# Performance work log

Hardware: AMD Instinct MI355X
Metric: run time of the kernel (lower is better)

## Reference

```python
import jax, jax.numpy as jnp
import numpy as np

N = 50000      # nodes
E = 800000     # edges (before self-loops)
F_IN = 256     # nfeat
HEADS = 8      # nhead
C1 = 16        # hidden_sizes (per-head channels of conv1)
NCLS = 40      # nclass
NEG_SLOPE = 0.2


def setup_inputs() -> dict:
    key = jax.random.key(0)
    ks = jax.random.split(key, 12)
    s = 0.1
    x = jax.random.normal(ks[0], (N, F_IN), dtype=jnp.float32)
    edge_index = jax.random.randint(ks[1], (2, E), 0, N, dtype=jnp.int64)
    edge_attr = jax.random.normal(ks[2], (E,), dtype=jnp.float32)  # unused by forward
    W1 = jax.random.normal(ks[3], (F_IN, HEADS * C1), dtype=jnp.float32) * s
    att_src1 = jax.random.normal(ks[4], (HEADS, C1), dtype=jnp.float32) * s
    att_dst1 = jax.random.normal(ks[5], (HEADS, C1), dtype=jnp.float32) * s
    b1 = jnp.zeros((HEADS * C1,), dtype=jnp.float32)
    W2 = jax.random.normal(ks[6], (HEADS * C1, NCLS), dtype=jnp.float32) * s
    att_src2 = jax.random.normal(ks[7], (1, NCLS), dtype=jnp.float32) * s
    att_dst2 = jax.random.normal(ks[8], (1, NCLS), dtype=jnp.float32) * s
    b2 = jnp.zeros((NCLS,), dtype=jnp.float32)
    return {"x": x, "edge_index": edge_index, "edge_attr": edge_attr,
            "W1": W1, "att_src1": att_src1, "att_dst1": att_dst1, "b1": b1,
            "W2": W2, "att_src2": att_src2, "att_dst2": att_dst2, "b2": b2}


def gat_layer(x, W, att_src, att_dst, bias, src, dst, concat):
    """PyG-style GATConv (eval mode, no dropout). src/dst include self-loops."""
    H, C = att_src.shape
    h = (x @ W).reshape(-1, H, C)                     # [N,H,C]
    a_src = (h * att_src[None]).sum(-1)               # [N,H]
    a_dst = (h * att_dst[None]).sum(-1)               # [N,H]
    e = jax.nn.leaky_relu(a_src[src] + a_dst[dst], NEG_SLOPE)  # [Etot,H]
    # segment softmax over destination neighborhoods
    m = jax.ops.segment_max(e, dst, num_segments=N)   # [N,H]
    m = jax.lax.stop_gradient(jnp.where(jnp.isfinite(m), m, 0.0))
    p = jnp.exp(e - m[dst])
    denom = jax.ops.segment_sum(p, dst, num_segments=N)
    alpha = p / (denom[dst] + 1e-16)                  # [Etot,H]
    out = jax.ops.segment_sum(alpha[:, :, None] * h[src], dst, num_segments=N)  # [N,H,C]
    out = out.reshape(-1, H * C) if concat else out.mean(axis=1)
    return out + bias


def reference(x, edge_index, edge_attr, W1, att_src1, att_dst1, b1, W2, att_src2, att_dst2, b2):
    # add self loops (PyG GATConv default)
    loops = jnp.arange(N, dtype=edge_index.dtype)
    src = jnp.concatenate([edge_index[0], loops])
    dst = jnp.concatenate([edge_index[1], loops])
    # eval mode: F.dropout is identity
    h = jax.nn.elu(gat_layer(x, W1, att_src1, att_dst1, b1, src, dst, concat=True))
    final = gat_layer(h, W2, att_src2, att_dst2, b2, src, dst, concat=False)
    return final, jax.nn.log_softmax(final, axis=1)
```

## Files before the change

### kernel.cpp

```cpp
#include <hip/hip_runtime.h>

#define NN 50000
#define EE 800000
#define FIN 256
#define HD 8
#define C1 16
#define HC 128
#define NC 40
#define NEG 0.2f
#define CAP 64
#define R2 32
#define BM 64
#define GB1 ((NN + BM - 1) / BM)
#define NP_N (NN / 8)
#define SCB 2048

typedef __attribute__((ext_vector_type(8))) short short8;
typedef __attribute__((ext_vector_type(4))) float f32x4;
union FragU { uint4 u; short8 s; };

__device__ __forceinline__ float leaky(float v){ return v > 0.f ? v : NEG * v; }

__device__ __forceinline__ unsigned int f2bf(float f){
  unsigned int u = __float_as_uint(f);
  u += 0x7fffu + ((u >> 16) & 1u);
  return u >> 16;
}
__device__ __forceinline__ unsigned int pack2bf(float a, float b){
  return f2bf(a) | (f2bf(b) << 16);
}
__device__ __forceinline__ float bflo(unsigned int u){ return __uint_as_float(u << 16); }
__device__ __forceinline__ float bfhi(unsigned int u){ return __uint_as_float(u & 0xffff0000u); }
__device__ __forceinline__ float bfus(unsigned short u){ return __uint_as_float((unsigned int)u << 16); }

__global__ __launch_bounds__(256) void k_prep(const float* __restrict__ W1,
                                              uint4* __restrict__ W1bfs,
                                              const int* __restrict__ ei,
                                              int* __restrict__ cnt,
                                              int* __restrict__ srcp){
  const int tid = threadIdx.x;
  if (blockIdx.x < 16){
    int f = blockIdx.x * 256 + tid;
    int lane = f & 63, nt = (f >> 6) & 7, kt = f >> 9;
    int quad = lane >> 4, l16 = lane & 15;
    const float* src = W1 + (size_t)(kt * 32 + quad * 8) * HC + nt * 16 + l16;
    unsigned int p[4];
#pragma unroll
    for (int jj = 0; jj < 4; jj++){
      float v0 = src[(size_t)(2 * jj) * HC];
      float v1 = src[(size_t)(2 * jj + 1) * HC];
      p[jj] = pack2bf(v0, v1);
    }
    W1bfs[f] = make_uint4(p[0], p[1], p[2], p[3]);
    return;
  }
  const int b = blockIdx.x - 16;
  const int part = b & 7, rank = b >> 3;
  const int lo = part * NP_N, hi = lo + NP_N;
  for (int e = rank * 256 + tid; e < EE; e += 256 * 256){
    int d = ei[EE + e];
    if (d >= lo && d < hi){
      int s = ei[e];
      int pos = atomicAdd(&cnt[d], 1);
      if (pos < CAP) srcp[d * CAP + pos] = s;
    }
  }
}

__global__ __launch_bounds__(256, 3) void k_gemm1(const float* __restrict__ x,
                                                  const uint4* __restrict__ W1bfs,
                                                  const float* __restrict__ att_s,
                                                  const float* __restrict__ att_d,
                                                  unsigned short* __restrict__ h1b,
                                                  float* __restrict__ as1,
                                                  float* __restrict__ ad1){
  const int tid = threadIdx.x;
  const int wave = tid >> 6, lane = tid & 63;
  const int quad = lane >> 4, l16 = lane & 15;
  const int m0 = blockIdx.x * BM + wave * 16;
  int arow = m0 + l16; if (arow >= NN) arow = NN - 1;
  const float* xr = x + (size_t)arow * FIN;

  float4 xa[16];
#pragma unroll
  for (int kt = 0; kt < 8; kt++){
    xa[2 * kt]     = *(const float4*)(xr + kt * 32 + quad * 8);
    xa[2 * kt + 1] = *(const float4*)(xr + kt * 32 + quad * 8 + 4);
  }
  FragU bf[8];
#pragma unroll
  for (int nt = 0; nt < 8; nt++) bf[nt].u = W1bfs[nt * 64 + lane];

  f32x4 acc[8];
#pragma unroll
  for (int t = 0; t < 8; t++) acc[t] = (f32x4){0.f, 0.f, 0.f, 0.f};

#pragma unroll
  for (int kt = 0; kt < 8; kt++){
    FragU bn[8];
    if (kt < 7){
#pragma unroll
      for (int nt = 0; nt < 8; nt++)
        bn[nt].u = W1bfs[((kt + 1) * 8 + nt) * 64 + lane];
    }
    FragU af;
    af.u = make_uint4(pack2bf(xa[2 * kt].x,     xa[2 * kt].y),
                      pack2bf(xa[2 * kt].z,     xa[2 * kt].w),
                      pack2bf(xa[2 * kt + 1].x, xa[2 * kt + 1].y),
                      pack2bf(xa[2 * kt + 1].z, xa[2 * kt + 1].w));
#pragma unroll
    for (int nt = 0; nt < 8; nt++)
      acc[nt] = __builtin_amdgcn_mfma_f32_16x16x32_bf16(af.s, bf[nt].s, acc[nt], 0, 0, 0);
    if (kt < 7){
#pragma unroll
      for (int nt = 0; nt < 8; nt++) bf[nt] = bn[nt];
    }
  }

  float sv[8], dv[8];
#pragma unroll
  for (int h = 0; h < 8; h++){ sv[h] = att_s[h * 16 + l16]; dv[h] = att_d[h * 16 + l16]; }
#pragma unroll
  for (int r = 0; r < 4; r++){
    const int gr = m0 + quad * 4 + r;
    float s[8], d[8];
#pragma unroll
    for (int h = 0; h < 8; h++){ s[h] = acc[h][r] * sv[h]; d[h] = acc[h][r] * dv[h]; }
#pragma unroll
    for (int o = 1; o < 16; o <<= 1){
#pragma unroll
      for (int h = 0; h < 8; h++){ s[h] += __shfl_xor(s[h], o); d[h] += __shfl_xor(d[h], o); }
    }
    if (gr < NN){
#pragma unroll
      for (int h = 0; h < 8; h++)
        h1b[(size_t)gr * HC + h * 16 + l16] = (unsigned short)f2bf(acc[h][r]);
      if (l16 == 0){
        *(float4*)(as1 + gr * 8)     = make_float4(s[0], s[1], s[2], s[3]);
        *(float4*)(as1 + gr * 8 + 4) = make_float4(s[4], s[5], s[6], s[7]);
        *(float4*)(ad1 + gr * 8)     = make_float4(d[0], d[1], d[2], d[3]);
        *(float4*)(ad1 + gr * 8 + 4) = make_float4(d[4], d[5], d[6], d[7]);
      }
    }
  }
}

__global__ __launch_bounds__(256) void k_agg1(const int* __restrict__ srcp,
                                              const int* __restrict__ cnt,
                                              const float* __restrict__ as1,
                                              const float* __restrict__ ad1,
                                              const unsigned short* __restrict__ h1b,
                                              const float* __restrict__ b1,
                                              unsigned short* __restrict__ h2b){
  __shared__ float wls[4][8][65];
  __shared__ int   sls[4][64];
  const int lane = threadIdx.x & 63, w = threadIdx.x >> 6;
  const int n = blockIdx.x * 4 + w;
  int deg = cnt[n]; if (deg > CAP - 1) deg = CAP - 1;
  const int nE = deg + 1;
  const bool act = (lane <= deg);
  int sA = n;
  if (lane < deg) sA = srcp[n * CAP + lane];
  const float4 d0 = *(const float4*)(ad1 + (size_t)n * 8);
  const float4 d1 = *(const float4*)(ad1 + (size_t)n * 8 + 4);
  const float4 a0 = *(const float4*)(as1 + (size_t)sA * 8);
  const float4 a1 = *(const float4*)(as1 + (size_t)sA * 8 + 4);
  float v[8];
  v[0]=leaky(a0.x+d0.x); v[1]=leaky(a0.y+d0.y); v[2]=leaky(a0.z+d0.z); v[3]=leaky(a0.w+d0.w);
  v[4]=leaky(a1.x+d1.x); v[5]=leaky(a1.y+d1.y); v[6]=leaky(a1.z+d1.z); v[7]=leaky(a1.w+d1.w);
#pragma unroll
  for (int h = 0; h < 8; h++) if (!act) v[h] = -3.0e38f;
  float mx[8];
#pragma unroll
  for (int h = 0; h < 8; h++) mx[h] = v[h];
#pragma unroll
  for (int o = 1; o < 64; o <<= 1){
#pragma unroll
    for (int h = 0; h < 8; h++) mx[h] = fmaxf(mx[h], __shfl_xor(mx[h], o));
  }
  float wt[8], den[8];
#pragma unroll
  for (int h = 0; h < 8; h++) wt[h] = act ? __expf(v[h] - mx[h]) : 0.f;
#pragma unroll
  for (int h = 0; h < 8; h++) den[h] = wt[h];
#pragma unroll
  for (int o = 1; o < 64; o <<= 1){
#pragma unroll
    for (int h = 0; h < 8; h++) den[h] += __shfl_xor(den[h], o);
  }
#pragma unroll
  for (int h = 0; h < 8; h++) wls[w][h][lane] = wt[h];
  sls[w][lane] = sA;
  __syncthreads();

  const int h = lane >> 3;
  float ax = 0.f, ay = 0.f;
  unsigned int u0, u1, u2, u3;
  float q0, q1, q2, q3;
  {
    const int i1 = min(1, deg), i2 = min(2, deg), i3 = min(3, deg);
    u0 = *(const unsigned int*)(h1b + (size_t)sls[w][0]  * HC + 2 * lane);
    u1 = *(const unsigned int*)(h1b + (size_t)sls[w][i1] * HC + 2 * lane);
    u2 = *(const unsigned int*)(h1b + (size_t)sls[w][i2] * HC + 2 * lane);
    u3 = *(const unsigned int*)(h1b + (size_t)sls[w][i3] * HC + 2 * lane);
    q0 = wls[w][h][0];
    q1 = (1 < nE) ? wls[w][h][1] : 0.f;
    q2 = (2 < nE) ? wls[w][h][2] : 0.f;
    q3 = (3 < nE) ? wls[w][h][3] : 0.f;
  }
  for (int i = 0; i < nE; i += 4){
    const int p0 = min(i + 4, deg), p1 = min(i + 5, deg);
    const int p2 = min(i + 6, deg), p3 = min(i + 7, deg);
    const unsigned int n0 = *(const unsigned int*)(h1b + (size_t)sls[w][p0] * HC + 2 * lane);
    const unsigned int n1 = *(const unsigned int*)(h1b + (size_t)sls[w][p1] * HC + 2 * lane);
    const unsigned int n2 = *(const unsigned int*)(h1b + (size_t)sls[w][p2] * HC + 2 * lane);
    const unsigned int n3 = *(const unsigned int*)(h1b + (size_t)sls[w][p3] * HC + 2 * lane);
    const float r0 = (i + 4 < nE) ? wls[w][h][p0] : 0.f;
    const float r1 = (i + 5 < nE) ? wls[w][h][p1] : 0.f;
    const float r2 = (i + 6 < nE) ? wls[w][h][p2] : 0.f;
    const float r3 = (i + 7 < nE) ? wls[w][h][p3] : 0.f;
    ax += q0 * bflo(u0); ay += q0 * bfhi(u0);
    ax += q1 * bflo(u1); ay += q1 * bfhi(u1);
    ax += q2 * bflo(u2); ay += q2 * bfhi(u2);
    ax += q3 * bflo(u3); ay += q3 * bfhi(u3);
    u0 = n0; u1 = n1; u2 = n2; u3 = n3;
    q0 = r0; q1 = r1; q2 = r2; q3 = r3;
  }
  const float invd = 1.f / (den[h] + 1e-16f);
  const float2 bb = *(const float2*)(b1 + 2 * lane);
  float ox = ax * invd + bb.x;
  float oy = ay * invd + bb.y;
  ox = ox > 0.f ? ox : (__expf(ox) - 1.f);
  oy = oy > 0.f ? oy : (__expf(oy) - 1.f);
  *(unsigned int*)(h2b + (size_t)n * HC + 2 * lane) = pack2bf(ox, oy);
}

__global__ __launch_bounds__(256) void k_gemm2(const unsigned short* __restrict__ h2b,
                                               const float* __restrict__ W2,
                                               const float* __restrict__ att_s2,
                                               const float* __restrict__ att_d2,
                                               unsigned short* __restrict__ gb,
                                               float* __restrict__ as2,
                                               float* __restrict__ ad2){
  __shared__ float hs[R2][HC + 2];
  __shared__ float w2s[HC * NC];
  const int tid = threadIdx.x;
  const int r0 = blockIdx.x * R2;
  for (int i = tid; i < HC * NC; i += 256) w2s[i] = W2[i];
  for (int i = tid; i < R2 * (HC / 2); i += 256){
    int r = i / (HC / 2), c = i % (HC / 2);
    unsigned int u = (r0 + r < NN) ? ((const unsigned int*)h2b)[(size_t)(r0 + r) * (HC / 2) + c] : 0u;
    hs[r][2 * c]     = bflo(u);
    hs[r][2 * c + 1] = bfhi(u);
  }
  __syncthreads();
  const int r = tid >> 3, j = tid & 7;
  float acc[5] = {0.f, 0.f, 0.f, 0.f, 0.f};
  for (int k = 0; k < HC; k++){
    float hv = hs[r][k];
#pragma unroll
    for (int q = 0; q < 5; q++) acc[q] += hv * w2s[k * NC + j + 8 * q];
  }
  const int node = r0 + r;
  if (node < NN){
    float s = 0.f, d = 0.f;
#pragma unroll
    for (int q = 0; q < 5; q++){
      int c = j + 8 * q;
      gb[(size_t)node * NC + c] = (unsigned short)f2bf(acc[q]);
      s += acc[q] * att_s2[c];
      d += acc[q] * att_d2[c];
    }
#pragma unroll
    for (int o = 1; o < 8; o <<= 1){ s += __shfl_xor(s, o); d += __shfl_xor(d, o); }
    if (j == 0){ as2[node] = s; ad2[node] = d; }
  }
}

__global__ __launch_bounds__(256) void k_agg2(const int* __restrict__ srcp,
                                              const int* __restrict__ cnt,
                                              const float* __restrict__ as2,
                                              const float* __restrict__ ad2,
                                              const unsigned short* __restrict__ gb,
                                              const float* __restrict__ b2,
                                              float* __restrict__ out){
  __shared__ float wls[4][64];
  __shared__ int   sls[4][64];
  const int lane = threadIdx.x & 63, w = threadIdx.x >> 6;
  const int n = blockIdx.x * 4 + w;
  int deg = cnt[n]; if (deg > CAP - 1) deg = CAP - 1;
  const int nE = deg + 1;
  const bool act = (lane <= deg);
  int sA = n;
  if (lane < deg) sA = srcp[n * CAP + lane];
  const float ad = ad2[n];
  float v = act ? leaky(as2[sA] + ad) : -3.0e38f;
  float mx = v;
#pragma unroll
  for (int o = 1; o < 64; o <<= 1) mx = fmaxf(mx, __shfl_xor(mx, o));
  float wt = act ? __expf(v - mx) : 0.f;
  float den = wt;
#pragma unroll
  for (int o = 1; o < 64; o <<= 1) den += __shfl_xor(den, o);
  wls[w][lane] = wt;
  sls[w][lane] = sA;
  __syncthreads();

  const int c = min(lane, NC - 1);
  float acc = 0.f;
  float g0, g1, g2, g3, q0, q1, q2, q3;
  {
    const int i1 = min(1, deg), i2 = min(2, deg), i3 = min(3, deg);
    g0 = bfus(gb[(size_t)sls[w][0]  * NC + c]);
    g1 = bfus(gb[(size_t)sls[w][i1] * NC + c]);
    g2 = bfus(gb[(size_t)sls[w][i2] * NC + c]);
    g3 = bfus(gb[(size_t)sls[w][i3] * NC + c]);
    q0 = wls[w][0];
    q1 = (1 < nE) ? wls[w][1] : 0.f;
    q2 = (2 < nE) ? wls[w][2] : 0.f;
    q3 = (3 < nE) ? wls[w][3] : 0.f;
  }
  for (int i = 0; i < nE; i += 4){
    const int p0 = min(i + 4, deg), p1 = min(i + 5, deg);
    const int p2 = min(i + 6, deg), p3 = min(i + 7, deg);
    const float h0 = bfus(gb[(size_t)sls[w][p0] * NC + c]);
    const float h1 = bfus(gb[(size_t)sls[w][p1] * NC + c]);
    const float h2 = bfus(gb[(size_t)sls[w][p2] * NC + c]);
    const float h3 = bfus(gb[(size_t)sls[w][p3] * NC + c]);
    const float r0 = (i + 4 < nE) ? wls[w][p0] : 0.f;
    const float r1 = (i + 5 < nE) ? wls[w][p1] : 0.f;
    const float r2 = (i + 6 < nE) ? wls[w][p2] : 0.f;
    const float r3 = (i + 7 < nE) ? wls[w][p3] : 0.f;
    acc += q0 * g0 + q1 * g1 + q2 * g2 + q3 * g3;
    g0 = h0; g1 = h1; g2 = h2; g3 = h3;
    q0 = r0; q1 = r1; q2 = r2; q3 = r3;
  }
  const float invd = 1.f / (den + 1e-16f);
  const bool cl = (lane < NC);
  float f = acc * invd + b2[c];
  if (cl) out[(size_t)n * NC + lane] = f;
  float fv = cl ? f : -3.4e38f;
  float m2 = fv;
#pragma unroll
  for (int o = 1; o < 64; o <<= 1) m2 = fmaxf(m2, __shfl_xor(m2, o));
  float ex = cl ? __expf(fv - m2) : 0.f;
#pragma unroll
  for (int o = 1; o < 64; o <<= 1) ex += __shfl_xor(ex, o);
  const float lse = m2 + __logf(ex);
  if (cl) out[(size_t)(NN * NC) + (size_t)n * NC + lane] = fv - lse;
}

extern "C" void kernel_launch(void* const* d_in, const int* in_sizes, int n_in,
                              void* d_out, int out_size, void* d_ws, size_t ws_size,
                              hipStream_t stream){
  const float* x      = (const float*)d_in[0];
  const int*   ei     = (const int*)  d_in[1];
  const float* W1     = (const float*)d_in[3];
  const float* att_s1 = (const float*)d_in[4];
  const float* att_d1 = (const float*)d_in[5];
  const float* b1     = (const float*)d_in[6];
  const float* W2     = (const float*)d_in[7];
  const float* att_s2 = (const float*)d_in[8];
  const float* att_d2 = (const float*)d_in[9];
  const float* b2     = (const float*)d_in[10];
  float* out = (float*)d_out;

  char* wp = (char*)d_ws;
  uint4* W1bfs = (uint4*)wp;                 wp += (size_t)4096 * 16;
  unsigned short* h1b = (unsigned short*)wp; wp += (size_t)NN * HC * 2;
  unsigned short* h2b = (unsigned short*)wp; wp += (size_t)NN * HC * 2;
  unsigned short* gb  = (unsigned short*)wp; wp += (size_t)NN * NC * 2;
  float* as1 = (float*)wp;                   wp += (size_t)NN * HD * 4;
  float* ad1 = (float*)wp;                   wp += (size_t)NN * HD * 4;
  float* as2 = (float*)wp;                   wp += (size_t)NN * 4;
  float* ad2 = (float*)wp;                   wp += (size_t)NN * 4;
  int* cnt   = (int*)wp;                     wp += (size_t)NN * 4;
  int* srcp  = (int*)wp;                     wp += (size_t)NN * CAP * 4;

  hipMemsetAsync(cnt, 0, (size_t)NN * sizeof(int), stream);
  k_prep  <<<16 + SCB, 256, 0, stream>>>(W1, W1bfs, ei, cnt, srcp);
  k_gemm1 <<<GB1, 256, 0, stream>>>(x, W1bfs, att_s1, att_d1, h1b, as1, ad1);
  k_agg1  <<<NN / 4, 256, 0, stream>>>(srcp, cnt, as1, ad1, h1b, b1, h2b);
  k_gemm2 <<<(NN + R2 - 1) / R2, 256, 0, stream>>>(h2b, W2, att_s2, att_d2, gb, as2, ad2);
  k_agg2  <<<NN / 4, 256, 0, stream>>>(srcp, cnt, as2, ad2, gb, b2, out);
}
```

Before: 291.4 us.

## Restructure GAT aggregation softmax per head-lane and batch neighbor gathers

In the layer-1 aggregation, the softmax changes layout: each lane now handles one head and a strided set of edges, so the reductions use three shuffles instead of full 64-lane butterflies over eight heads. Edge scores are staged in LDS as [edge][head]. In both aggregation kernels the neighbor feature gathers are restructured: the first 16 are issued at once, and the rest go in batches of 8, to expose more memory-level parallelism. The block-wide __syncthreads is removed, since each wavefront only touches its own LDS slice. This relies on intra-wavefront LDS ordering and raises register pressure from the wider unrolled gathers.

```diff
diff --git a/kernel.cpp b/kernel.cpp
--- a/kernel.cpp
+++ b/kernel.cpp
@@ -152,81 +152,69 @@
                                               const unsigned short* __restrict__ h1b,
                                               const float* __restrict__ b1,
                                               unsigned short* __restrict__ h2b){
-  __shared__ float wls[4][8][65];
+  __shared__ float wls[4][64][8];
   __shared__ int   sls[4][64];
   const int lane = threadIdx.x & 63, w = threadIdx.x >> 6;
   const int n = blockIdx.x * 4 + w;
   int deg = cnt[n]; if (deg > CAP - 1) deg = CAP - 1;
   const int nE = deg + 1;
-  const bool act = (lane <= deg);
   int sA = n;
   if (lane < deg) sA = srcp[n * CAP + lane];
-  const float4 d0 = *(const float4*)(ad1 + (size_t)n * 8);
-  const float4 d1 = *(const float4*)(ad1 + (size_t)n * 8 + 4);
-  const float4 a0 = *(const float4*)(as1 + (size_t)sA * 8);
-  const float4 a1 = *(const float4*)(as1 + (size_t)sA * 8 + 4);
-  float v[8];
-  v[0]=leaky(a0.x+d0.x); v[1]=leaky(a0.y+d0.y); v[2]=leaky(a0.z+d0.z); v[3]=leaky(a0.w+d0.w);
-  v[4]=leaky(a1.x+d1.x); v[5]=leaky(a1.y+d1.y); v[6]=leaky(a1.z+d1.z); v[7]=leaky(a1.w+d1.w);
-#pragma unroll
-  for (int h = 0; h < 8; h++) if (!act) v[h] = -3.0e38f;
-  float mx[8];
-#pragma unroll
-  for (int h = 0; h < 8; h++) mx[h] = v[h];
-#pragma unroll
-  for (int o = 1; o < 64; o <<= 1){
-#pragma unroll
-    for (int h = 0; h < 8; h++) mx[h] = fmaxf(mx[h], __shfl_xor(mx[h], o));
-  }
-  float wt[8], den[8];
-#pragma unroll
-  for (int h = 0; h < 8; h++) wt[h] = act ? __expf(v[h] - mx[h]) : 0.f;
-#pragma unroll
-  for (int h = 0; h < 8; h++) den[h] = wt[h];
-#pragma unroll
-  for (int o = 1; o < 64; o <<= 1){
-#pragma unroll
-    for (int h = 0; h < 8; h++) den[h] += __shfl_xor(den[h], o);
-  }
-#pragma unroll
-  for (int h = 0; h < 8; h++) wls[w][h][lane] = wt[h];
   sls[w][lane] = sA;
-  __syncthreads();
-
-  const int h = lane >> 3;
+
+  const int h = lane >> 3, e8 = lane & 7;
+  const float adg = ad1[n * 8 + h];
+  int nCh = (nE + 7) >> 3; if (nCh < 2) nCh = 2;
+
+  float mx = -3.0e38f;
+  for (int c = 0; c < nCh; c++){
+    const int i = c * 8 + e8;
+    const int s = sls[w][i];
+    const float v = (i < nE) ? leaky(as1[(size_t)s * 8 + h] + adg) : -3.0e38f;
+    wls[w][i][h] = v;
+    mx = fmaxf(mx, v);
+  }
+  mx = fmaxf(mx, __shfl_xor(mx, 1));
+  mx = fmaxf(mx, __shfl_xor(mx, 2));
+  mx = fmaxf(mx, __shfl_xor(mx, 4));
+
+  float den = 0.f;
+  for (int c = 0; c < nCh; c++){
+    const int i = c * 8 + e8;
+    const float v = wls[w][i][h];
+    const float wt = (i < nE) ? __expf(v - mx) : 0.f;
+    wls[w][i][h] = wt;
+    den += wt;
+  }
+  den += __shfl_xor(den, 1);
+  den += __shfl_xor(den, 2);
+  den += __shfl_xor(den, 4);
+
+  const unsigned int* hp = (const unsigned int*)h1b;
   float ax = 0.f, ay = 0.f;
-  unsigned int u0, u1, u2, u3;
-  float q0, q1, q2, q3;
   {
-    const int i1 = min(1, deg), i2 = min(2, deg), i3 = min(3, deg);
-    u0 = *(const unsigned int*)(h1b + (size_t)sls[w][0]  * HC + 2 * lane);
-    u1 = *(const unsigned int*)(h1b + (size_t)sls[w][i1] * HC + 2 * lane);
-    u2 = *(const unsigned int*)(h1b + (size_t)sls[w][i2] * HC + 2 * lane);
-    u3 = *(const unsigned int*)(h1b + (size_t)sls[w][i3] * HC + 2 * lane);
-    q0 = wls[w][h][0];
-    q1 = (1 < nE) ? wls[w][h][1] : 0.f;
-    q2 = (2 < nE) ? wls[w][h][2] : 0.f;
-    q3 = (3 < nE) ? wls[w][h][3] : 0.f;
-  }
-  for (int i = 0; i < nE; i += 4){
-    const int p0 = min(i + 4, deg), p1 = min(i + 5, deg);
-    const int p2 = min(i + 6, deg), p3 = min(i + 7, deg);
-    const unsigned int n0 = *(const unsigned int*)(h1b + (size_t)sls[w][p0] * HC + 2 * lane);
-    const unsigned int n1 = *(const unsigned int*)(h1b + (size_t)sls[w][p1] * HC + 2 * lane);
-    const unsigned int n2 = *(const unsigned int*)(h1b + (size_t)sls[w][p2] * HC + 2 * lane);
-    const unsigned int n3 = *(const unsigned int*)(h1b + (size_t)sls[w][p3] * HC + 2 * lane);
-    const float r0 = (i + 4 < nE) ? wls[w][h][p0] : 0.f;
-    const float r1 = (i + 5 < nE) ? wls[w][h][p1] : 0.f;
-    const float r2 = (i + 6 < nE) ? wls[w][h][p2] : 0.f;
-    const float r3 = (i + 7 < nE) ? wls[w][h][p3] : 0.f;
-    ax += q0 * bflo(u0); ay += q0 * bfhi(u0);
-    ax += q1 * bflo(u1); ay += q1 * bfhi(u1);
-    ax += q2 * bflo(u2); ay += q2 * bfhi(u2);
-    ax += q3 * bflo(u3); ay += q3 * bfhi(u3);
-    u0 = n0; u1 = n1; u2 = n2; u3 = n3;
-    q0 = r0; q1 = r1; q2 = r2; q3 = r3;
-  }
-  const float invd = 1.f / (den[h] + 1e-16f);
+    unsigned int u[16]; float q[16];
+#pragma unroll
+    for (int i = 0; i < 16; i++){
+      u[i] = hp[(size_t)(unsigned)((sls[w][i] << 6) + lane)];
+      q[i] = wls[w][i][h];
+    }
+#pragma unroll
+    for (int i = 0; i < 16; i++){ ax += q[i] * bflo(u[i]); ay += q[i] * bfhi(u[i]); }
+  }
+  for (int i0 = 16; i0 < nE; i0 += 8){
+    unsigned int uu[8]; float qq[8];
+#pragma unroll
+    for (int t = 0; t < 8; t++){
+      const int j = i0 + t, p = min(j, deg);
+      uu[t] = hp[(size_t)(unsigned)((sls[w][p] << 6) + lane)];
+      qq[t] = (j < nE) ? wls[w][p][h] : 0.f;
+    }
+#pragma unroll
+    for (int t = 0; t < 8; t++){ ax += qq[t] * bflo(uu[t]); ay += qq[t] * bfhi(uu[t]); }
+  }
+
+  const float invd = 1.f / (den + 1e-16f);
   const float2 bb = *(const float2*)(b1 + 2 * lane);
   float ox = ax * invd + bb.x;
   float oy = ay * invd + bb.y;
@@ -293,6 +281,7 @@
   const bool act = (lane <= deg);
   int sA = n;
   if (lane < deg) sA = srcp[n * CAP + lane];
+  sls[w][lane] = sA;
   const float ad = ad2[n];
   float v = act ? leaky(as2[sA] + ad) : -3.0e38f;
   float mx = v;
@@ -303,37 +292,29 @@
 #pragma unroll
   for (int o = 1; o < 64; o <<= 1) den += __shfl_xor(den, o);
   wls[w][lane] = wt;
-  sls[w][lane] = sA;
-  __syncthreads();
 
   const int c = min(lane, NC - 1);
   float acc = 0.f;
-  float g0, g1, g2, g3, q0, q1, q2, q3;
   {
-    const int i1 = min(1, deg), i2 = min(2, deg), i3 = min(3, deg);
-    g0 = bfus(gb[(size_t)sls[w][0]  * NC + c]);
-    g1 = bfus(gb[(size_t)sls[w][i1] * NC + c]);
-    g2 = bfus(gb[(size_t)sls[w][i2] * NC + c]);
-    g3 = bfus(gb[(size_t)sls[w][i3] * NC + c]);
-    q0 = wls[w][0];
-    q1 = (1 < nE) ? wls[w][1] : 0.f;
-    q2 = (2 < nE) ? wls[w][2] : 0.f;
-    q3 = (3 < nE) ? wls[w][3] : 0.f;
-  }
-  for (int i = 0; i < nE; i += 4){
-    const int p0 = min(i + 4, deg), p1 = min(i + 5, deg);
-    const int p2 = min(i + 6, deg), p3 = min(i + 7, deg);
-    const float h0 = bfus(gb[(size_t)sls[w][p0] * NC + c]);
-    const float h1 = bfus(gb[(size_t)sls[w][p1] * NC + c]);
-    const float h2 = bfus(gb[(size_t)sls[w][p2] * NC + c]);
-    const float h3 = bfus(gb[(size_t)sls[w][p3] * NC + c]);
-    const float r0 = (i + 4 < nE) ? wls[w][p0] : 0.f;
-    const float r1 = (i + 5 < nE) ? wls[w][p1] : 0.f;
-    const float r2 = (i + 6 < nE) ? wls[w][p2] : 0.f;
-    const float r3 = (i + 7 < nE) ? wls[w][p3] : 0.f;
-    acc += q0 * g0 + q1 * g1 + q2 * g2 + q3 * g3;
-    g0 = h0; g1 = h1; g2 = h2; g3 = h3;
-    q0 = r0; q1 = r1; q2 = r2; q3 = r3;
+    float g[16], q[16];
+#pragma unroll
+    for (int i = 0; i < 16; i++){
+      g[i] = bfus(gb[(size_t)(unsigned)(sls[w][i] * NC + c)]);
+      q[i] = wls[w][i];
+    }
+#pragma unroll
+    for (int i = 0; i < 16; i++) acc += q[i] * g[i];
+  }
+  for (int i0 = 16; i0 < nE; i0 += 8){
+    float gg[8], qq[8];
+#pragma unroll
+    for (int t = 0; t < 8; t++){
+      const int j = i0 + t;
+      gg[t] = bfus(gb[(size_t)(unsigned)(sls[w][j] * NC + c)]);
+      qq[t] = wls[w][j];
+    }
+#pragma unroll
+    for (int t = 0; t < 8; t++) acc += qq[t] * gg[t];
   }
   const float invd = 1.f / (den + 1e-16f);
   const bool cl = (lane < NC);
```

New measurement: 259.8 us. 10.8% less time.
